# Optimization experiments

Hardware: AMD Instinct MI355X
Metric: run time of the kernel (lower is better)

The kernel has to match this reference:

```python
import jax, jax.numpy as jnp
import numpy as np
import math

B, S, L, D, H, F = 4, 1024, 4, 256, 8, 1024
NUM_LETTERS = 22
VOCAB = NUM_LETTERS + 3
HD = D // H
DISSONANCE = 0.5


def setup_inputs() -> dict:
    key = jax.random.key(0)
    ks = iter(jax.random.split(key, 64))
    r = lambda shape, s=0.05: jax.random.normal(next(ks), shape, dtype=jnp.float32) * s
    inp = {
        'input_roots': jax.random.randint(next(ks), (B, S, 3), 0, VOCAB),
        'gematria': jax.random.uniform(next(ks), (B, S), dtype=jnp.float32),
        'letter_embed': r((VOCAB, D), 0.02),
        'root_proj_w': r((3 * D, D)), 'root_proj_b': jnp.zeros((D,)),
        'root_ln_g': jnp.ones((D,)), 'root_ln_b': jnp.zeros((D,)),
        'input_proj_w': r((2 * D, D)), 'input_proj_b': jnp.zeros((D,)),
        'input_ln_g': jnp.ones((D,)), 'input_ln_b': jnp.zeros((D,)),
        'qw': r((L, D, D)), 'qb': jnp.zeros((L, D)),
        'kw': r((L, D, D)), 'kb': jnp.zeros((L, D)),
        'vw': r((L, D, D)), 'vb': jnp.zeros((L, D)),
        'ow': r((L, D, D)), 'ob': jnp.zeros((L, D)),
        'dist_scale': r((L, H), 0.1), 'diss_sens': jnp.full((L, H), 0.5),
        'ff1w': r((L, D, F)), 'ff1b': jnp.zeros((L, F)),
        'ff2w': r((L, F, D)), 'ff2b': jnp.zeros((L, D)),
        'ln1g': jnp.ones((L, D)), 'ln1b': jnp.zeros((L, D)),
        'ln2g': jnp.ones((L, D)), 'ln2b': jnp.zeros((L, D)),
        'out_ln_g': jnp.ones((D,)), 'out_ln_b': jnp.zeros((D,)),
        'h1w': r((D, NUM_LETTERS)), 'h1b': jnp.zeros((NUM_LETTERS,)),
        'h2w': r((D, NUM_LETTERS)), 'h2b': jnp.zeros((NUM_LETTERS,)),
        'h3w': r((D, NUM_LETTERS)), 'h3b': jnp.zeros((NUM_LETTERS,)),
    }
    return inp


def _ln(x, g, b):
    m = jnp.mean(x, -1, keepdims=True)
    v = jnp.mean(jnp.square(x - m), -1, keepdims=True)
    return (x - m) * jax.lax.rsqrt(v + 1e-5) * g + b


def _rtl_pos(s, d):
    # flipped sinusoidal PE: token j gets original position s-1-j
    pos = (s - 1 - jnp.arange(s, dtype=jnp.float32))[:, None]
    div = jnp.exp(jnp.arange(0, d, 2, dtype=jnp.float32) * (-(math.log(10000.0) / d)))
    pe = jnp.zeros((s, d))
    pe = pe.at[:, 0::2].set(jnp.sin(pos * div))
    pe = pe.at[:, 1::2].set(jnp.cos(pos * div))
    return pe


def _forward(input_roots, gematria, letter_embed, root_proj_w, root_proj_b,
             root_ln_g, root_ln_b, input_proj_w, input_proj_b, input_ln_g, input_ln_b,
             qw, qb, kw, kb, vw, vb, ow, ob, dist_scale, diss_sens,
             ff1w, ff1b, ff2w, ff2b, ln1g, ln1b, ln2g, ln2b,
             out_ln_g, out_ln_b, h1w, h1b, h2w, h2b, h3w, h3b):
    b, s, _ = input_roots.shape
    # root encoder
    letters = letter_embed[input_roots]                      # (b,s,3,D)
    root_emb = _ln(letters.reshape(b, s, 3 * D) @ root_proj_w + root_proj_b, root_ln_g, root_ln_b)
    # gematria sinusoidal
    angles = (gematria[..., None] * 500.0) * jnp.exp(
        jnp.arange(0, D, 2, dtype=jnp.float32) * (-(math.log(10000.0) / D)))
    gem_emb = jnp.concatenate([jnp.sin(angles), jnp.cos(angles)], axis=-1)  # (b,s,D)
    x = jnp.concatenate([root_emb, gem_emb], axis=-1) @ input_proj_w + input_proj_b
    x = _ln(x + _rtl_pos(s, D)[None], input_ln_g, input_ln_b)
    # distance matrix |i-j| shared across layers
    pos = jnp.arange(s, dtype=jnp.float32)
    dist = jnp.abs(pos[None, :] - pos[:, None])              # (s,s)
    scale = 1.0 / math.sqrt(HD)
    for i in range(L):
        normed = _ln(x, ln1g[i], ln1b[i])
        Q = (normed @ qw[i] + qb[i]).reshape(b, s, H, HD)
        K = (normed @ kw[i] + kb[i]).reshape(b, s, H, HD)
        V = (normed @ vw[i] + vb[i]).reshape(b, s, H, HD)
        scores = jnp.einsum('bqhd,bkhd->bhqk', Q, K) * scale
        penalty = dist_scale[i] * (1.0 - DISSONANCE * diss_sens[i])  # (H,)
        bias = -jnp.abs(penalty)[:, None, None] * dist[None]         # (H,s,s)
        attn = jax.nn.softmax(scores + bias[None], axis=-1)
        out = jnp.einsum('bhqk,bkhd->bqhd', attn, V).reshape(b, s, D)
        x = x + (out @ ow[i] + ob[i])
        h = _ln(x, ln2g[i], ln2b[i])
        x = x + (jax.nn.gelu(h @ ff1w[i] + ff1b[i], approximate=False) @ ff2w[i] + ff2b[i])
    x = _ln(x, out_ln_g, out_ln_b)
    return (x @ h1w + h1b, x @ h2w + h2b, x @ h3w + h3b)


def reference(input_roots, gematria, letter_embed, root_proj_w, root_proj_b,
              root_ln_g, root_ln_b, input_proj_w, input_proj_b, input_ln_g, input_ln_b,
              qw, qb, kw, kb, vw, vb, ow, ob, dist_scale, diss_sens,
              ff1w, ff1b, ff2w, ff2b, ln1g, ln1b, ln2g, ln2b,
              out_ln_g, out_ln_b, h1w, h1b, h2w, h2b, h3w, h3b):
    return _forward(input_roots, gematria, letter_embed, root_proj_w, root_proj_b,
                    root_ln_g, root_ln_b, input_proj_w, input_proj_b, input_ln_g, input_ln_b,
                    qw, qb, kw, kb, vw, vb, ow, ob, dist_scale, diss_sens,
                    ff1w, ff1b, ff2w, ff2b, ln1g, ln1b, ln2g, ln2b,
                    out_ln_g, out_ln_b, h1w, h1b, h2w, h2b, h3w, h3b)
```

## Files before the change

### kernel.cpp

```cpp
#include <hip/hip_runtime.h>
#include <hip/hip_bf16.h>
#include <math.h>

#define NTOK   4096
#define SEQ    1024
#define DMODEL 256
#define NHEAD  8
#define FDIM   1024
#define NLAYER 4

typedef __attribute__((ext_vector_type(8))) short short8v;
typedef __attribute__((ext_vector_type(4))) float f32x4;

#define LDS3(p) ((__attribute__((address_space(3))) unsigned int*)(p))
#define GAS1(p) ((const __attribute__((address_space(1))) unsigned int*)(p))

__device__ __forceinline__ void gl_lds16(const void* g, void* l) {
    __builtin_amdgcn_global_load_lds(GAS1(g), LDS3(l), 16, 0, 0);
}
__device__ __forceinline__ short f2bf(float v) {
    __hip_bfloat16 h = __float2bfloat16(v);
    return __builtin_bit_cast(short, h);
}

__device__ __forceinline__ void blockSum2(float& s1, float& s2, float* red) {
    #pragma unroll
    for (int off = 32; off > 0; off >>= 1) {
        s1 += __shfl_down(s1, off);
        s2 += __shfl_down(s2, off);
    }
    int lane = threadIdx.x & 63, w = threadIdx.x >> 6;
    __syncthreads();
    if (lane == 0) { red[w] = s1; red[4 + w] = s2; }
    __syncthreads();
    s1 = red[0] + red[1] + red[2] + red[3];
    s2 = red[4] + red[5] + red[6] + red[7];
}

struct TD { const float* src; __hip_bfloat16* dst; int K; int M; };
struct TDs { TD d[29]; };

__global__ __launch_bounds__(256) void transpose_kernel(TDs p) {
    __shared__ float ld[32][33];
    TD d = p.d[blockIdx.y];
    int tm = (d.M + 31) >> 5;
    int kt = blockIdx.x / tm, mt = blockIdx.x % tm;
    if (kt * 32 >= d.K) return;
    int tx = threadIdx.x & 31, ty = threadIdx.x >> 5;
    #pragma unroll
    for (int r = 0; r < 4; ++r) {
        int k = kt * 32 + ty + r * 8, m = mt * 32 + tx;
        if (m < d.M) ld[ty + r * 8][tx] = d.src[(long)k * d.M + m];
    }
    __syncthreads();
    #pragma unroll
    for (int r = 0; r < 4; ++r) {
        int m = mt * 32 + ty + r * 8, k = kt * 32 + tx;
        if (m < d.M) d.dst[(long)m * d.K + k] = __float2bfloat16(ld[tx][ty + r * 8]);
    }
}

template <int TM, int TN, int EPI>
__global__ __launch_bounds__(256) void mm_kernel(
    const __hip_bfloat16* __restrict__ A, const __hip_bfloat16* __restrict__ Bw,
    const float* __restrict__ bias, float* __restrict__ Cf,
    __hip_bfloat16* __restrict__ Cb, int N, int K, int M,
    const float* __restrict__ b2, const float* __restrict__ b3,
    __hip_bfloat16* __restrict__ Ck, __hip_bfloat16* __restrict__ Cv)
{
    constexpr int BK = 64;
    __shared__ __align__(16) short As[2][TM * BK];
    __shared__ __align__(16) short Bs[2][TN * BK];
    const int tid = threadIdx.x;
    const int lane = tid & 63, wid = tid >> 6;
    const int wr = wid >> 1, wc = wid & 1;
    const int n0 = blockIdx.y * TM, m0 = blockIdx.x * TN;
    const int l15 = lane & 15, g = lane >> 4;
    constexpr int FM = (TM / 32 > 0) ? TM / 32 : 1;
    constexpr int FN = TN / 32;
    f32x4 acc[FM][FN] = {};
    const int nt = K >> 6;

    auto stage = [&](int buf, int k0) {
        constexpr int CA = TM * 8;
        #pragma unroll
        for (int j = 0; j < (CA + 255) / 256; ++j) {
            int cid = tid + j * 256;
            if (CA % 256 == 0 || cid < CA) {
                int r = cid >> 3, sl = cid & 7, ss = sl ^ (r & 7);
                gl_lds16(A + (long)(n0 + r) * K + k0 + ss * 8, (char*)As[buf] + cid * 16);
            }
        }
        constexpr int CB = TN * 8;
        #pragma unroll
        for (int j = 0; j < CB / 256; ++j) {
            int cid = tid + j * 256;
            int r = cid >> 3, sl = cid & 7, ss = sl ^ (r & 7);
            gl_lds16(Bw + (long)(m0 + r) * K + k0 + ss * 8, (char*)Bs[buf] + cid * 16);
        }
    };

    stage(0, 0);
    __syncthreads();
    for (int t = 0; t < nt; ++t) {
        int cur = t & 1;
        if (t + 1 < nt) stage(cur ^ 1, (t + 1) * BK);
        #pragma unroll
        for (int ks = 0; ks < 2; ++ks) {
            short8v af[FM], bfr[FN];
            #pragma unroll
            for (int mi = 0; mi < FM; ++mi) {
                int row = wr * (TM / 2) + mi * 16 + l15;
                int slot = (ks * 4 + g) ^ (row & 7);
                af[mi] = *(const short8v*)((const char*)As[cur] + row * (BK * 2) + slot * 16);
            }
            #pragma unroll
            for (int ni = 0; ni < FN; ++ni) {
                int row = wc * (TN / 2) + ni * 16 + l15;
                int slot = (ks * 4 + g) ^ (row & 7);
                bfr[ni] = *(const short8v*)((const char*)Bs[cur] + row * (BK * 2) + slot * 16);
            }
            #pragma unroll
            for (int mi = 0; mi < FM; ++mi)
                #pragma unroll
                for (int ni = 0; ni < FN; ++ni)
                    acc[mi][ni] = __builtin_amdgcn_mfma_f32_16x16x32_bf16(
                        af[mi], bfr[ni], acc[mi][ni], 0, 0, 0);
        }
        __syncthreads();
    }

    #pragma unroll
    for (int mi = 0; mi < FM; ++mi) {
        #pragma unroll
        for (int ni = 0; ni < FN; ++ni) {
            int colb = m0 + wc * (TN / 2) + ni * 16 + l15;
            float bv;
            if (EPI == 6) bv = (colb < 256) ? bias[colb] : (colb < 512) ? b2[colb - 256] : b3[colb - 512];
            else bv = bias[colb];
            if (EPI == 6 && colb >= 512) {
                int c2 = colb - 512;
                int h = c2 >> 5, dd = c2 & 31;
                int row0 = n0 + wr * (TM / 2) + mi * 16 + g * 4;
                int bb = row0 >> 10, ss = row0 & 1023;
                short4 pk;
                pk.x = f2bf(acc[mi][ni][0] + bv);
                pk.y = f2bf(acc[mi][ni][1] + bv);
                pk.z = f2bf(acc[mi][ni][2] + bv);
                pk.w = f2bf(acc[mi][ni][3] + bv);
                *(short4*)((short*)Cv + ((long)((bb * 8 + h) * 32 + dd) << 10) + ss) = pk;
            } else {
                #pragma unroll
                for (int i = 0; i < 4; ++i) {
                    int row = n0 + wr * (TM / 2) + mi * 16 + g * 4 + i;
                    float v = acc[mi][ni][i] + bv;
                    if (EPI == 0) Cf[(long)row * M + colb] = v;
                    else if (EPI == 2) {
                        v = 0.5f * v * (1.f + erff(v * 0.70710678f));
                        Cb[(long)row * M + colb] = __float2bfloat16(v);
                    } else if (EPI == 5) {
                        if (colb < 66) {
                            int hd = colb / 22, jj = colb - hd * 22;
                            Cf[(long)hd * (NTOK * 22) + (long)row * 22 + jj] = v;
                        }
                    } else if (EPI == 6) {
                        __hip_bfloat16* dst = (colb < 256) ? Cb : Ck;
                        int cc = (colb < 256) ? colb : colb - 256;
                        dst[(long)row * 256 + cc] = __float2bfloat16(v);
                    }
                }
            }
        }
    }
}

__global__ __launch_bounds__(256) void mm_wide_ln_kernel(
    const __hip_bfloat16* __restrict__ A, const __hip_bfloat16* __restrict__ Bw,
    const float* __restrict__ bias, float* __restrict__ xio,
    __hip_bfloat16* __restrict__ nrm, const float* __restrict__ lng,
    const float* __restrict__ lnb, int K)
{
    constexpr int BK = 64;
    __shared__ __align__(16) short As[2][16 * BK];
    __shared__ __align__(16) short Bs[2][256 * BK];
    __shared__ float2 red2[4][16];
    const int tid = threadIdx.x;
    const int lane = tid & 63, wid = tid >> 6;
    const int l15 = lane & 15, g = lane >> 4;
    const int n0 = blockIdx.x * 16;
    f32x4 acc[4] = {};
    const int nt = K >> 6;

    auto stage = [&](int buf, int k0) {
        if (tid < 128) {
            int r = tid >> 3, sl = tid & 7, ss = sl ^ (r & 7);
            gl_lds16(A + (long)(n0 + r) * K + k0 + ss * 8, (char*)As[buf] + tid * 16);
        }
        #pragma unroll
        for (int j = 0; j < 8; ++j) {
            int cid = tid + j * 256;
            int r = cid >> 3, sl = cid & 7, ss = sl ^ (r & 7);
            gl_lds16(Bw + (long)r * K + k0 + ss * 8, (char*)Bs[buf] + cid * 16);
        }
    };

    stage(0, 0);
    __syncthreads();
    for (int t = 0; t < nt; ++t) {
        int cur = t & 1;
        if (t + 1 < nt) stage(cur ^ 1, (t + 1) * BK);
        #pragma unroll
        for (int ks = 0; ks < 2; ++ks) {
            short8v af;
            {
                int slot = (ks * 4 + g) ^ (l15 & 7);
                af = *(const short8v*)((const char*)As[cur] + l15 * (BK * 2) + slot * 16);
            }
            #pragma unroll
            for (int ni = 0; ni < 4; ++ni) {
                int brow = wid * 64 + ni * 16 + l15;
                int slot = (ks * 4 + g) ^ (brow & 7);
                short8v bfr = *(const short8v*)((const char*)Bs[cur] + brow * (BK * 2) + slot * 16);
                acc[ni] = __builtin_amdgcn_mfma_f32_16x16x32_bf16(af, bfr, acc[ni], 0, 0, 0);
            }
        }
        __syncthreads();
    }

    float pvt[4][4];
    float rs[4] = {0.f, 0.f, 0.f, 0.f}, rq[4] = {0.f, 0.f, 0.f, 0.f};
    #pragma unroll
    for (int ni = 0; ni < 4; ++ni) {
        int col = wid * 64 + ni * 16 + l15;
        float bv = bias[col];
        #pragma unroll
        for (int i = 0; i < 4; ++i) {
            int row = n0 + g * 4 + i;
            float v = acc[ni][i] + bv + xio[(long)row * 256 + col];
            pvt[ni][i] = v;
            rs[i] += v;
            rq[i] += v * v;
        }
    }
    #pragma unroll
    for (int i = 0; i < 4; ++i) {
        #pragma unroll
        for (int off = 8; off; off >>= 1) {
            rs[i] += __shfl_xor(rs[i], off);
            rq[i] += __shfl_xor(rq[i], off);
        }
    }
    __syncthreads();
    if (l15 == 0) {
        #pragma unroll
        for (int i = 0; i < 4; ++i)
            red2[wid][g * 4 + i] = make_float2(rs[i], rq[i]);
    }
    __syncthreads();
    #pragma unroll
    for (int i = 0; i < 4; ++i) {
        int lr = g * 4 + i;
        float s1 = red2[0][lr].x + red2[1][lr].x + red2[2][lr].x + red2[3][lr].x;
        float s2 = red2[0][lr].y + red2[1][lr].y + red2[2][lr].y + red2[3][lr].y;
        float mean = s1 * (1.f / 256.f);
        float var = s2 * (1.f / 256.f) - mean * mean;
        float rsx = rsqrtf(var + 1e-5f);
        int row = n0 + lr;
        #pragma unroll
        for (int ni = 0; ni < 4; ++ni) {
            int col = wid * 64 + ni * 16 + l15;
            float v = pvt[ni][i];
            xio[(long)row * 256 + col] = v;
            nrm[(long)row * 256 + col] =
                __float2bfloat16((v - mean) * rsx * lng[col] + lnb[col]);
        }
    }
}

__global__ __launch_bounds__(256) void attn_mfma_kernel(
    const __hip_bfloat16* __restrict__ Q, const __hip_bfloat16* __restrict__ Kx,
    const __hip_bfloat16* __restrict__ Vt, __hip_bfloat16* __restrict__ Oa,
    const float* __restrict__ dsc, const float* __restrict__ dss)
{
    __shared__ __align__(16) short Qs[64 * 32];
    __shared__ __align__(16) short Ks[2][64 * 32];
    __shared__ __align__(16) short Vs[2][32 * 64];
    __shared__ __align__(16) short Ps[4 * 16 * 64];
    const int tid = threadIdx.x, lane = tid & 63, wid = tid >> 6;
    const int qt = blockIdx.x, bh = blockIdx.y, b = bh >> 3, h = bh & 7;
    const float pen = fabsf(dsc[h] * (1.f - 0.5f * dss[h]));
    const int l15 = lane & 15, g = lane >> 4;
    const float scale = 0.17677669529663689f;

    auto stageKV = [&](int buf, int kt) {
        int r = tid >> 2, sl = tid & 3, ss = sl ^ (r & 3);
        gl_lds16(Kx + ((long)(b * SEQ + kt * 64 + r) * DMODEL + h * 32) + ss * 8,
                 (char*)Ks[buf] + tid * 16);
        int d = tid >> 3, sl8 = tid & 7, ss8 = sl8 ^ (d & 7);
        gl_lds16(Vt + ((long)(bh * 32 + d) << 10) + kt * 64 + ss8 * 8,
                 (char*)Vs[buf] + tid * 16);
    };

    {
        int r = tid >> 2, sl = tid & 3, ss = sl ^ (r & 3);
        gl_lds16(Q + ((long)(b * SEQ + qt * 64 + r) * DMODEL + h * 32) + ss * 8,
                 (char*)Qs + tid * 16);
    }
    stageKV(0, 0);
    __syncthreads();

    short8v bq;
    {
        int row = wid * 16 + l15;
        int slot = g ^ (row & 3);
        bq = *(const short8v*)((const char*)Qs + row * 64 + slot * 16);
    }

    float m = -1e30f, l = 0.f;
    f32x4 oacc[2] = {};
    const float qpos = (float)(qt * 64 + wid * 16 + l15);
    char* pbase = (char*)Ps + wid * 2048 + l15 * 128;

    for (int kt = 0; kt < 16; ++kt) {
        int cur = kt & 1;
        if (kt < 15) stageKV(cur ^ 1, kt + 1);

        float s[4][4];
        float smax = -1e30f;
        #pragma unroll
        for (int ni = 0; ni < 4; ++ni) {
            int krow = ni * 16 + l15;
            int slot = g ^ (krow & 3);
            short8v ak = *(const short8v*)((const char*)Ks[cur] + krow * 64 + slot * 16);
            f32x4 z = {0.f, 0.f, 0.f, 0.f};
            f32x4 sa = __builtin_amdgcn_mfma_f32_16x16x32_bf16(ak, bq, z, 0, 0, 0);
            float kbase = (float)(kt * 64 + ni * 16 + g * 4);
            #pragma unroll
            for (int i = 0; i < 4; ++i) {
                float v = sa[i] * scale - pen * fabsf(qpos - (kbase + (float)i));
                s[ni][i] = v;
                smax = fmaxf(smax, v);
            }
        }
        smax = fmaxf(smax, __shfl_xor(smax, 16));
        smax = fmaxf(smax, __shfl_xor(smax, 32));
        float mn = fmaxf(m, smax);
        float fac = __expf(m - mn);
        m = mn;
        float ps = 0.f;
        #pragma unroll
        for (int ni = 0; ni < 4; ++ni) {
            short4 pk;
            #pragma unroll
            for (int i = 0; i < 4; ++i) {
                float p = __expf(s[ni][i] - mn);
                ps += p;
                ((short*)&pk)[i] = f2bf(p);
            }
            int slot = (ni * 2 + (g >> 1)) ^ (l15 & 7);
            *(short4*)(pbase + slot * 16 + (g & 1) * 8) = pk;
        }
        ps += __shfl_xor(ps, 16);
        ps += __shfl_xor(ps, 32);
        l = l * fac + ps;

        float facr[4];
        #pragma unroll
        for (int i = 0; i < 4; ++i) facr[i] = __shfl(fac, g * 4 + i);
        #pragma unroll
        for (int n2 = 0; n2 < 2; ++n2)
            #pragma unroll
            for (int i = 0; i < 4; ++i) oacc[n2][i] *= facr[i];

        #pragma unroll
        for (int ks = 0; ks < 2; ++ks) {
            int slot = (ks * 4 + g) ^ (l15 & 7);
            short8v pa = *(const short8v*)(pbase + slot * 16);
            #pragma unroll
            for (int n2 = 0; n2 < 2; ++n2) {
                int d = n2 * 16 + l15;
                int vslot = (ks * 4 + g) ^ (d & 7);
                short8v vb = *(const short8v*)((const char*)Vs[cur] + d * 128 + vslot * 16);
                oacc[n2] = __builtin_amdgcn_mfma_f32_16x16x32_bf16(pa, vb, oacc[n2], 0, 0, 0);
            }
        }
        __syncthreads();
    }
    float lr[4];
    #pragma unroll
    for (int i = 0; i < 4; ++i) lr[i] = __shfl(l, g * 4 + i);
    #pragma unroll
    for (int n2 = 0; n2 < 2; ++n2) {
        #pragma unroll
        for (int i = 0; i < 4; ++i) {
            float v = oacc[n2][i] / lr[i];
            long row = b * SEQ + qt * 64 + wid * 16 + g * 4 + i;
            Oa[row * DMODEL + h * 32 + n2 * 16 + l15] = __float2bfloat16(v);
        }
    }
}

__global__ __launch_bounds__(256) void gather_kernel(
    const int* __restrict__ roots, const float* __restrict__ letE,
    __hip_bfloat16* __restrict__ cat,
    const float* __restrict__ h1b, const float* __restrict__ h2b,
    const float* __restrict__ h3b, float* __restrict__ biascat)
{
    const int n = blockIdx.x, t = threadIdx.x;
    int r0 = roots[n * 3 + 0], r1 = roots[n * 3 + 1], r2 = roots[n * 3 + 2];
    cat[(long)n * 768 + t]       = __float2bfloat16(letE[r0 * DMODEL + t]);
    cat[(long)n * 768 + 256 + t] = __float2bfloat16(letE[r1 * DMODEL + t]);
    cat[(long)n * 768 + 512 + t] = __float2bfloat16(letE[r2 * DMODEL + t]);
    if (n == 0 && t < 66)
        biascat[t] = (t < 22) ? h1b[t] : (t < 44) ? h2b[t - 22] : h3b[t - 44];
}

__global__ __launch_bounds__(256) void ln_gem_kernel(
    const float* __restrict__ tmpf, const float* __restrict__ gem,
    const float* __restrict__ gg, const float* __restrict__ gb,
    __hip_bfloat16* __restrict__ catin)
{
    __shared__ float red[8];
    const int n = blockIdx.x, t = threadIdx.x;
    const float LC = 0.0359778921f;
    float v = tmpf[(long)n * DMODEL + t];
    float s1 = v, s2 = v * v;
    blockSum2(s1, s2, red);
    float mean = s1 * (1.f / 256.f);
    float var = s2 * (1.f / 256.f) - mean * mean;
    catin[(long)n * 512 + t] =
        __float2bfloat16((v - mean) * rsqrtf(var + 1e-5f) * gg[t] + gb[t]);
    float gv = gem[n];
    int j = (t < 128) ? t : t - 128;
    float ang = gv * 500.f * expf(-(float)(2 * j) * LC);
    catin[(long)n * 512 + 256 + t] = __float2bfloat16((t < 128) ? sinf(ang) : cosf(ang));
}

__global__ __launch_bounds__(256) void ln_pe2_kernel(
    const float* __restrict__ tmpf, const float* __restrict__ gg,
    const float* __restrict__ gb, const float* __restrict__ g1,
    const float* __restrict__ b1, float* __restrict__ x,
    __hip_bfloat16* __restrict__ nrm)
{
    __shared__ float red[8];
    const int n = blockIdx.x, t = threadIdx.x;
    const int s = n & (SEQ - 1);
    const float LC = 0.0359778921f;
    float pos = (float)(SEQ - 1 - s);
    float dv = expf(-(float)(t & ~1) * LC);
    float pe = (t & 1) ? cosf(pos * dv) : sinf(pos * dv);
    float v = tmpf[(long)n * DMODEL + t] + pe;
    float s1 = v, s2 = v * v;
    blockSum2(s1, s2, red);
    float mean = s1 * (1.f / 256.f);
    float var = s2 * (1.f / 256.f) - mean * mean;
    float xv = (v - mean) * rsqrtf(var + 1e-5f) * gg[t] + gb[t];
    x[(long)n * DMODEL + t] = xv;
    s1 = xv; s2 = xv * xv;
    blockSum2(s1, s2, red);
    mean = s1 * (1.f / 256.f);
    var = s2 * (1.f / 256.f) - mean * mean;
    nrm[(long)n * DMODEL + t] =
        __float2bfloat16((xv - mean) * rsqrtf(var + 1e-5f) * g1[t] + b1[t]);
}

extern "C" void kernel_launch(void* const* d_in, const int* in_sizes, int n_in,
                              void* d_out, int out_size, void* d_ws, size_t ws_size,
                              hipStream_t stream)
{
    const int*   roots = (const int*)  d_in[0];
    const float* gem   = (const float*)d_in[1];
    const float* letE  = (const float*)d_in[2];
    const float* rpw   = (const float*)d_in[3];
    const float* rpb   = (const float*)d_in[4];
    const float* rlg   = (const float*)d_in[5];
    const float* rlb   = (const float*)d_in[6];
    const float* ipw   = (const float*)d_in[7];
    const float* ipb   = (const float*)d_in[8];
    const float* ilg   = (const float*)d_in[9];
    const float* ilb   = (const float*)d_in[10];
    const float* qw    = (const float*)d_in[11];
    const float* qb    = (const float*)d_in[12];
    const float* kw    = (const float*)d_in[13];
    const float* kb    = (const float*)d_in[14];
    const float* vw    = (const float*)d_in[15];
    const float* vb    = (const float*)d_in[16];
    const float* ow    = (const float*)d_in[17];
    const float* ob    = (const float*)d_in[18];
    const float* dsc   = (const float*)d_in[19];
    const float* dss   = (const float*)d_in[20];
    const float* ff1w  = (const float*)d_in[21];
    const float* ff1b  = (const float*)d_in[22];
    const float* ff2w  = (const float*)d_in[23];
    const float* ff2b  = (const float*)d_in[24];
    const float* ln1g  = (const float*)d_in[25];
    const float* ln1b  = (const float*)d_in[26];
    const float* ln2g  = (const float*)d_in[27];
    const float* ln2b  = (const float*)d_in[28];
    const float* olng  = (const float*)d_in[29];
    const float* olnb  = (const float*)d_in[30];
    const float* h1w   = (const float*)d_in[31];
    const float* h1b   = (const float*)d_in[32];
    const float* h2w   = (const float*)d_in[33];
    const float* h2b   = (const float*)d_in[34];
    const float* h3w   = (const float*)d_in[35];
    const float* h3b   = (const float*)d_in[36];

    char* wsb = (char*)d_ws;
    float*          x    = (float*)         (wsb + (0l  << 20));
    float*          tmpf = (float*)         (wsb + (4l  << 20));
    __hip_bfloat16* nrm  = (__hip_bfloat16*)(wsb + (8l  << 20));
    __hip_bfloat16* qbuf = (__hip_bfloat16*)(wsb + (10l << 20));
    __hip_bfloat16* kbuf = (__hip_bfloat16*)(wsb + (12l << 20));
    __hip_bfloat16* vtb  = (__hip_bfloat16*)(wsb + (14l << 20));
    __hip_bfloat16* aob  = (__hip_bfloat16*)(wsb + (16l << 20));
    __hip_bfloat16* hbb  = (__hip_bfloat16*)(wsb + (18l << 20));
    __hip_bfloat16* catb  = hbb;
    __hip_bfloat16* catin = qbuf;
    __hip_bfloat16* wb   = (__hip_bfloat16*)(wsb + (26l << 20));
    float*          biascat = (float*)      (wsb + (34l << 20));

    __hip_bfloat16* rpw_t  = wb;
    __hip_bfloat16* ipw_t  = wb + 196608;
    __hip_bfloat16* qkv_t  = wb + 327680;
    __hip_bfloat16* ow_t   = wb + 1114112;
    __hip_bfloat16* ff1w_t = wb + 1376256;
    __hip_bfloat16* ff2w_t = wb + 2424832;
    __hip_bfloat16* head_t = wb + 3473408;

    hipMemsetAsync(head_t, 0, 32768 * 2, stream);

    TDs td;
    td.d[0] = {rpw, rpw_t, 768, 256};
    td.d[1] = {ipw, ipw_t, 512, 256};
    for (int l = 0; l < 4; ++l) {
        td.d[2 + l]  = {qw + l * 65536,  qkv_t + l * 196608 + 0,      256, 256};
        td.d[6 + l]  = {kw + l * 65536,  qkv_t + l * 196608 + 65536,  256, 256};
        td.d[10 + l] = {vw + l * 65536,  qkv_t + l * 196608 + 131072, 256, 256};
        td.d[14 + l] = {ow + l * 65536,  ow_t + l * 65536,  256, 256};
        td.d[18 + l] = {ff1w + l * 262144, ff1w_t + l * 262144, 256, 1024};
        td.d[22 + l] = {ff2w + l * 262144, ff2w_t + l * 262144, 1024, 256};
    }
    td.d[26] = {h1w, head_t + 0 * 22 * 256, 256, 22};
    td.d[27] = {h2w, head_t + 1 * 22 * 256, 256, 22};
    td.d[28] = {h3w, head_t + 2 * 22 * 256, 256, 22};
    transpose_kernel<<<dim3(256, 29), 256, 0, stream>>>(td);

    gather_kernel<<<NTOK, 256, 0, stream>>>(roots, letE, catb, h1b, h2b, h3b, biascat);
    mm_kernel<32, 64, 0><<<dim3(4, 128), 256, 0, stream>>>(
        catb, rpw_t, rpb, tmpf, nullptr, NTOK, 768, 256, nullptr, nullptr, nullptr, nullptr);
    ln_gem_kernel<<<NTOK, 256, 0, stream>>>(tmpf, gem, rlg, rlb, catin);
    mm_kernel<32, 64, 0><<<dim3(4, 128), 256, 0, stream>>>(
        catin, ipw_t, ipb, tmpf, nullptr, NTOK, 512, 256, nullptr, nullptr, nullptr, nullptr);
    ln_pe2_kernel<<<NTOK, 256, 0, stream>>>(tmpf, ilg, ilb, ln1g, ln1b, x, nrm);

    for (int l = 0; l < NLAYER; ++l) {
        mm_kernel<64, 64, 6><<<dim3(12, 64), 256, 0, stream>>>(
            nrm, qkv_t + l * 196608, qb + l * 256, nullptr, qbuf, NTOK, 256, 768,
            kb + l * 256, vb + l * 256, kbuf, vtb);
        attn_mfma_kernel<<<dim3(16, 32), 256, 0, stream>>>(qbuf, kbuf, vtb, aob,
                                                           dsc + l * 8, dss + l * 8);
        mm_wide_ln_kernel<<<dim3(NTOK / 16), 256, 0, stream>>>(
            aob, ow_t + l * 65536, ob + l * 256, x, nrm,
            ln2g + l * 256, ln2b + l * 256, 256);
        mm_kernel<64, 64, 2><<<dim3(16, 64), 256, 0, stream>>>(
            nrm, ff1w_t + l * 262144, ff1b + l * 1024, nullptr, hbb, NTOK, 256, 1024,
            nullptr, nullptr, nullptr, nullptr);
        const float* ng = (l == 3) ? olng : ln1g + (l + 1) * 256;
        const float* nb = (l == 3) ? olnb : ln1b + (l + 1) * 256;
        mm_wide_ln_kernel<<<dim3(NTOK / 16), 256, 0, stream>>>(
            hbb, ff2w_t + l * 262144, ff2b + l * 256, x, nrm, ng, nb, 1024);
    }
    mm_kernel<32, 64, 5><<<dim3(2, 128), 256, 0, stream>>>(
        nrm, head_t, biascat, (float*)d_out, nullptr, NTOK, 256, 128,
        nullptr, nullptr, nullptr, nullptr);
}
```

Baseline: 435.0 us.

## Fuse embedding LayerNorms into wide GEMMs and restructure attention with key-range skipping

Replaces the two embedding GEMMs and their separate LayerNorm/sinusoid kernels with wide 16-row GEMM kernels that apply bias, LayerNorm, the gematria encoding and the positional encoding in the epilogue. This drops the fp32 intermediate buffer and two extra launches. Attention now runs one 64-thread wave per 16 query rows, loading K and V fragments straight from global memory instead of staging them through shared memory. It also limits the key tiles to the range where the distance penalty stays above -30. The transpose kernel writes zero padding for the head weights, so the separate memset is gone. The key-range bound relies on the penalty being positive and skips terms that are tiny but not exactly zero; the new attention layout gives up shared-memory reuse of K and V across waves.

```diff
diff --git a/kernel.cpp b/kernel.cpp
--- a/kernel.cpp
+++ b/kernel.cpp
@@ -23,27 +23,13 @@
     return __builtin_bit_cast(short, h);
 }
 
-__device__ __forceinline__ void blockSum2(float& s1, float& s2, float* red) {
-    #pragma unroll
-    for (int off = 32; off > 0; off >>= 1) {
-        s1 += __shfl_down(s1, off);
-        s2 += __shfl_down(s2, off);
-    }
-    int lane = threadIdx.x & 63, w = threadIdx.x >> 6;
-    __syncthreads();
-    if (lane == 0) { red[w] = s1; red[4 + w] = s2; }
-    __syncthreads();
-    s1 = red[0] + red[1] + red[2] + red[3];
-    s2 = red[4] + red[5] + red[6] + red[7];
-}
-
-struct TD { const float* src; __hip_bfloat16* dst; int K; int M; };
+struct TD { const float* src; __hip_bfloat16* dst; int K; int M; int Mpad; };
 struct TDs { TD d[29]; };
 
 __global__ __launch_bounds__(256) void transpose_kernel(TDs p) {
     __shared__ float ld[32][33];
     TD d = p.d[blockIdx.y];
-    int tm = (d.M + 31) >> 5;
+    int tm = (d.Mpad + 31) >> 5;
     int kt = blockIdx.x / tm, mt = blockIdx.x % tm;
     if (kt * 32 >= d.K) return;
     int tx = threadIdx.x & 31, ty = threadIdx.x >> 5;
@@ -57,6 +43,7 @@
     for (int r = 0; r < 4; ++r) {
         int m = mt * 32 + ty + r * 8, k = kt * 32 + tx;
         if (m < d.M) d.dst[(long)m * d.K + k] = __float2bfloat16(ld[tx][ty + r * 8]);
+        else if (m < d.Mpad) d.dst[(long)m * d.K + k] = __float2bfloat16(0.f);
     }
 }
 
@@ -174,61 +161,99 @@
     }
 }
 
+#define WIDE_GEMM_BODY(Abuf, Bwp, Kval)                                           \
+    constexpr int BK = 64;                                                        \
+    const int tid = threadIdx.x;                                                  \
+    const int lane = tid & 63, wid = tid >> 6;                                    \
+    const int l15 = lane & 15, g = lane >> 4;                                     \
+    const int n0 = blockIdx.x * 16;                                               \
+    f32x4 acc[4] = {};                                                            \
+    const int nt = (Kval) >> 6;                                                   \
+    auto stage = [&](int buf, int k0) {                                           \
+        if (tid < 128) {                                                          \
+            int r = tid >> 3, sl = tid & 7, ss = sl ^ (r & 7);                    \
+            gl_lds16((Abuf) + (long)(n0 + r) * (Kval) + k0 + ss * 8,              \
+                     (char*)As[buf] + tid * 16);                                  \
+        }                                                                         \
+        _Pragma("unroll")                                                         \
+        for (int j = 0; j < 8; ++j) {                                             \
+            int cid = tid + j * 256;                                              \
+            int r = cid >> 3, sl = cid & 7, ss = sl ^ (r & 7);                    \
+            gl_lds16((Bwp) + (long)r * (Kval) + k0 + ss * 8,                      \
+                     (char*)Bs[buf] + cid * 16);                                  \
+        }                                                                         \
+    };                                                                            \
+    stage(0, 0);                                                                  \
+    __syncthreads();                                                              \
+    for (int t = 0; t < nt; ++t) {                                                \
+        int cur = t & 1;                                                          \
+        if (t + 1 < nt) stage(cur ^ 1, (t + 1) * BK);                             \
+        _Pragma("unroll")                                                         \
+        for (int ks = 0; ks < 2; ++ks) {                                          \
+            short8v af;                                                           \
+            {                                                                     \
+                int slot = (ks * 4 + g) ^ (l15 & 7);                              \
+                af = *(const short8v*)((const char*)As[cur] + l15 * (BK * 2) + slot * 16); \
+            }                                                                     \
+            _Pragma("unroll")                                                     \
+            for (int ni = 0; ni < 4; ++ni) {                                      \
+                int brow = wid * 64 + ni * 16 + l15;                              \
+                int slot = (ks * 4 + g) ^ (brow & 7);                             \
+                short8v bfr = *(const short8v*)((const char*)Bs[cur] + brow * (BK * 2) + slot * 16); \
+                acc[ni] = __builtin_amdgcn_mfma_f32_16x16x32_bf16(af, bfr, acc[ni], 0, 0, 0); \
+            }                                                                     \
+        }                                                                         \
+        __syncthreads();                                                          \
+    }
+
+__device__ __forceinline__ void wide_rowstats(
+    float pvt[4][4], float2 red2[4][16], int wid, int l15, int g,
+    float mean[4], float rstd[4])
+{
+    float rs[4] = {0.f, 0.f, 0.f, 0.f}, rq[4] = {0.f, 0.f, 0.f, 0.f};
+    #pragma unroll
+    for (int ni = 0; ni < 4; ++ni)
+        #pragma unroll
+        for (int i = 0; i < 4; ++i) { rs[i] += pvt[ni][i]; rq[i] += pvt[ni][i] * pvt[ni][i]; }
+    #pragma unroll
+    for (int i = 0; i < 4; ++i) {
+        #pragma unroll
+        for (int off = 8; off; off >>= 1) {
+            rs[i] += __shfl_xor(rs[i], off);
+            rq[i] += __shfl_xor(rq[i], off);
+        }
+    }
+    __syncthreads();
+    if (l15 == 0) {
+        #pragma unroll
+        for (int i = 0; i < 4; ++i)
+            red2[wid][g * 4 + i] = make_float2(rs[i], rq[i]);
+    }
+    __syncthreads();
+    #pragma unroll
+    for (int i = 0; i < 4; ++i) {
+        int lr = g * 4 + i;
+        float s1 = red2[0][lr].x + red2[1][lr].x + red2[2][lr].x + red2[3][lr].x;
+        float s2 = red2[0][lr].y + red2[1][lr].y + red2[2][lr].y + red2[3][lr].y;
+        float mn = s1 * (1.f / 256.f);
+        float var = s2 * (1.f / 256.f) - mn * mn;
+        mean[i] = mn;
+        rstd[i] = rsqrtf(var + 1e-5f);
+    }
+}
+
 __global__ __launch_bounds__(256) void mm_wide_ln_kernel(
     const __hip_bfloat16* __restrict__ A, const __hip_bfloat16* __restrict__ Bw,
     const float* __restrict__ bias, float* __restrict__ xio,
     __hip_bfloat16* __restrict__ nrm, const float* __restrict__ lng,
     const float* __restrict__ lnb, int K)
 {
-    constexpr int BK = 64;
-    __shared__ __align__(16) short As[2][16 * BK];
-    __shared__ __align__(16) short Bs[2][256 * BK];
+    __shared__ __align__(16) short As[2][16 * 64];
+    __shared__ __align__(16) short Bs[2][256 * 64];
     __shared__ float2 red2[4][16];
-    const int tid = threadIdx.x;
-    const int lane = tid & 63, wid = tid >> 6;
-    const int l15 = lane & 15, g = lane >> 4;
-    const int n0 = blockIdx.x * 16;
-    f32x4 acc[4] = {};
-    const int nt = K >> 6;
-
-    auto stage = [&](int buf, int k0) {
-        if (tid < 128) {
-            int r = tid >> 3, sl = tid & 7, ss = sl ^ (r & 7);
-            gl_lds16(A + (long)(n0 + r) * K + k0 + ss * 8, (char*)As[buf] + tid * 16);
-        }
-        #pragma unroll
-        for (int j = 0; j < 8; ++j) {
-            int cid = tid + j * 256;
-            int r = cid >> 3, sl = cid & 7, ss = sl ^ (r & 7);
-            gl_lds16(Bw + (long)r * K + k0 + ss * 8, (char*)Bs[buf] + cid * 16);
-        }
-    };
-
-    stage(0, 0);
-    __syncthreads();
-    for (int t = 0; t < nt; ++t) {
-        int cur = t & 1;
-        if (t + 1 < nt) stage(cur ^ 1, (t + 1) * BK);
-        #pragma unroll
-        for (int ks = 0; ks < 2; ++ks) {
-            short8v af;
-            {
-                int slot = (ks * 4 + g) ^ (l15 & 7);
-                af = *(const short8v*)((const char*)As[cur] + l15 * (BK * 2) + slot * 16);
-            }
-            #pragma unroll
-            for (int ni = 0; ni < 4; ++ni) {
-                int brow = wid * 64 + ni * 16 + l15;
-                int slot = (ks * 4 + g) ^ (brow & 7);
-                short8v bfr = *(const short8v*)((const char*)Bs[cur] + brow * (BK * 2) + slot * 16);
-                acc[ni] = __builtin_amdgcn_mfma_f32_16x16x32_bf16(af, bfr, acc[ni], 0, 0, 0);
-            }
-        }
-        __syncthreads();
-    }
+    WIDE_GEMM_BODY(A, Bw, K)
 
     float pvt[4][4];
-    float rs[4] = {0.f, 0.f, 0.f, 0.f}, rq[4] = {0.f, 0.f, 0.f, 0.f};
     #pragma unroll
     for (int ni = 0; ni < 4; ++ni) {
         int col = wid * 64 + ni * 16 + l15;
@@ -236,104 +261,171 @@
         #pragma unroll
         for (int i = 0; i < 4; ++i) {
             int row = n0 + g * 4 + i;
-            float v = acc[ni][i] + bv + xio[(long)row * 256 + col];
-            pvt[ni][i] = v;
-            rs[i] += v;
-            rq[i] += v * v;
-        }
-    }
+            pvt[ni][i] = acc[ni][i] + bv + xio[(long)row * 256 + col];
+        }
+    }
+    float mean[4], rstd[4];
+    wide_rowstats(pvt, red2, wid, l15, g, mean, rstd);
     #pragma unroll
     for (int i = 0; i < 4; ++i) {
-        #pragma unroll
-        for (int off = 8; off; off >>= 1) {
-            rs[i] += __shfl_xor(rs[i], off);
-            rq[i] += __shfl_xor(rq[i], off);
-        }
-    }
-    __syncthreads();
-    if (l15 == 0) {
-        #pragma unroll
-        for (int i = 0; i < 4; ++i)
-            red2[wid][g * 4 + i] = make_float2(rs[i], rq[i]);
-    }
-    __syncthreads();
-    #pragma unroll
-    for (int i = 0; i < 4; ++i) {
-        int lr = g * 4 + i;
-        float s1 = red2[0][lr].x + red2[1][lr].x + red2[2][lr].x + red2[3][lr].x;
-        float s2 = red2[0][lr].y + red2[1][lr].y + red2[2][lr].y + red2[3][lr].y;
-        float mean = s1 * (1.f / 256.f);
-        float var = s2 * (1.f / 256.f) - mean * mean;
-        float rsx = rsqrtf(var + 1e-5f);
-        int row = n0 + lr;
+        int row = n0 + g * 4 + i;
         #pragma unroll
         for (int ni = 0; ni < 4; ++ni) {
             int col = wid * 64 + ni * 16 + l15;
             float v = pvt[ni][i];
             xio[(long)row * 256 + col] = v;
             nrm[(long)row * 256 + col] =
-                __float2bfloat16((v - mean) * rsx * lng[col] + lnb[col]);
-        }
-    }
-}
-
-__global__ __launch_bounds__(256) void attn_mfma_kernel(
+                __float2bfloat16((v - mean[i]) * rstd[i] * lng[col] + lnb[col]);
+        }
+    }
+}
+
+__global__ __launch_bounds__(256) void wide_gem_kernel(
+    const __hip_bfloat16* __restrict__ A, const __hip_bfloat16* __restrict__ Bw,
+    const float* __restrict__ bias, const float* __restrict__ lng,
+    const float* __restrict__ lnb, const float* __restrict__ gem,
+    __hip_bfloat16* __restrict__ catin)
+{
+    __shared__ __align__(16) short As[2][16 * 64];
+    __shared__ __align__(16) short Bs[2][256 * 64];
+    __shared__ float2 red2[4][16];
+    WIDE_GEMM_BODY(A, Bw, 768)
+
+    const float LC = 0.0359778921f;
+    float pvt[4][4];
+    #pragma unroll
+    for (int ni = 0; ni < 4; ++ni) {
+        int col = wid * 64 + ni * 16 + l15;
+        float bv = bias[col];
+        #pragma unroll
+        for (int i = 0; i < 4; ++i) pvt[ni][i] = acc[ni][i] + bv;
+    }
+    float mean[4], rstd[4];
+    wide_rowstats(pvt, red2, wid, l15, g, mean, rstd);
+    float gv[4];
+    #pragma unroll
+    for (int i = 0; i < 4; ++i) gv[i] = gem[n0 + g * 4 + i];
+    #pragma unroll
+    for (int ni = 0; ni < 4; ++ni) {
+        int col = wid * 64 + ni * 16 + l15;
+        int j = col & 127;
+        float c = 500.f * __expf(-(float)(2 * j) * LC);
+        #pragma unroll
+        for (int i = 0; i < 4; ++i) {
+            int row = n0 + g * 4 + i;
+            catin[(long)row * 512 + col] = __float2bfloat16(
+                (pvt[ni][i] - mean[i]) * rstd[i] * lng[col] + lnb[col]);
+            float ang = gv[i] * c;
+            float gval = (col < 128) ? __sinf(ang) : __cosf(ang);
+            catin[(long)row * 512 + 256 + col] = __float2bfloat16(gval);
+        }
+    }
+}
+
+__global__ __launch_bounds__(256) void wide_pe_kernel(
+    const __hip_bfloat16* __restrict__ A, const __hip_bfloat16* __restrict__ Bw,
+    const float* __restrict__ bias, const float* __restrict__ lng,
+    const float* __restrict__ lnb, const float* __restrict__ g1,
+    const float* __restrict__ b1, float* __restrict__ x,
+    __hip_bfloat16* __restrict__ nrm)
+{
+    __shared__ __align__(16) short As[2][16 * 64];
+    __shared__ __align__(16) short Bs[2][256 * 64];
+    __shared__ float2 red2[4][16];
+    WIDE_GEMM_BODY(A, Bw, 512)
+
+    const float LC = 0.0359778921f;
+    float pvt[4][4];
+    #pragma unroll
+    for (int ni = 0; ni < 4; ++ni) {
+        int col = wid * 64 + ni * 16 + l15;
+        float bv = bias[col];
+        float dv = __expf(-(float)(col & ~1) * LC);
+        #pragma unroll
+        for (int i = 0; i < 4; ++i) {
+            int row = n0 + g * 4 + i;
+            float pos = (float)(1023 - (row & 1023));
+            float pe = (col & 1) ? __cosf(pos * dv) : __sinf(pos * dv);
+            pvt[ni][i] = acc[ni][i] + bv + pe;
+        }
+    }
+    float mean[4], rstd[4];
+    wide_rowstats(pvt, red2, wid, l15, g, mean, rstd);
+    #pragma unroll
+    for (int ni = 0; ni < 4; ++ni) {
+        int col = wid * 64 + ni * 16 + l15;
+        #pragma unroll
+        for (int i = 0; i < 4; ++i) {
+            float xv = (pvt[ni][i] - mean[i]) * rstd[i] * lng[col] + lnb[col];
+            pvt[ni][i] = xv;
+            x[(long)(n0 + g * 4 + i) * 256 + col] = xv;
+        }
+    }
+    __syncthreads();
+    wide_rowstats(pvt, red2, wid, l15, g, mean, rstd);
+    #pragma unroll
+    for (int ni = 0; ni < 4; ++ni) {
+        int col = wid * 64 + ni * 16 + l15;
+        #pragma unroll
+        for (int i = 0; i < 4; ++i) {
+            int row = n0 + g * 4 + i;
+            nrm[(long)row * 256 + col] = __float2bfloat16(
+                (pvt[ni][i] - mean[i]) * rstd[i] * g1[col] + b1[col]);
+        }
+    }
+}
+
+__global__ __launch_bounds__(64) void attn_mfma_kernel(
     const __hip_bfloat16* __restrict__ Q, const __hip_bfloat16* __restrict__ Kx,
     const __hip_bfloat16* __restrict__ Vt, __hip_bfloat16* __restrict__ Oa,
     const float* __restrict__ dsc, const float* __restrict__ dss)
 {
-    __shared__ __align__(16) short Qs[64 * 32];
-    __shared__ __align__(16) short Ks[2][64 * 32];
-    __shared__ __align__(16) short Vs[2][32 * 64];
-    __shared__ __align__(16) short Ps[4 * 16 * 64];
-    const int tid = threadIdx.x, lane = tid & 63, wid = tid >> 6;
-    const int qt = blockIdx.x, bh = blockIdx.y, b = bh >> 3, h = bh & 7;
+    __shared__ __align__(16) short Ps[16 * 64];
+    const int lane = threadIdx.x;
+    const int qt = blockIdx.x;
+    const int bh = blockIdx.y, b = bh >> 3, h = bh & 7;
+    const int l15 = lane & 15, g = lane >> 4;
     const float pen = fabsf(dsc[h] * (1.f - 0.5f * dss[h]));
-    const int l15 = lane & 15, g = lane >> 4;
     const float scale = 0.17677669529663689f;
 
-    auto stageKV = [&](int buf, int kt) {
-        int r = tid >> 2, sl = tid & 3, ss = sl ^ (r & 3);
-        gl_lds16(Kx + ((long)(b * SEQ + kt * 64 + r) * DMODEL + h * 32) + ss * 8,
-                 (char*)Ks[buf] + tid * 16);
-        int d = tid >> 3, sl8 = tid & 7, ss8 = sl8 ^ (d & 7);
-        gl_lds16(Vt + ((long)(bh * 32 + d) << 10) + kt * 64 + ss8 * 8,
-                 (char*)Vs[buf] + tid * 16);
-    };
-
-    {
-        int r = tid >> 2, sl = tid & 3, ss = sl ^ (r & 3);
-        gl_lds16(Q + ((long)(b * SEQ + qt * 64 + r) * DMODEL + h * 32) + ss * 8,
-                 (char*)Qs + tid * 16);
-    }
-    stageKV(0, 0);
-    __syncthreads();
-
-    short8v bq;
-    {
-        int row = wid * 16 + l15;
-        int slot = g ^ (row & 3);
-        bq = *(const short8v*)((const char*)Qs + row * 64 + slot * 16);
-    }
+    short8v bq = *(const short8v*)(Q + ((long)(b * SEQ + qt * 16 + l15) * DMODEL + h * 32 + g * 8));
 
     float m = -1e30f, l = 0.f;
     f32x4 oacc[2] = {};
-    const float qpos = (float)(qt * 64 + wid * 16 + l15);
-    char* pbase = (char*)Ps + wid * 2048 + l15 * 128;
-
-    for (int kt = 0; kt < 16; ++kt) {
-        int cur = kt & 1;
-        if (kt < 15) stageKV(cur ^ 1, kt + 1);
+    const float qpos = (float)(qt * 16 + l15);
+    char* pbase = (char*)Ps + l15 * 128;
+
+    int klo = 0, khi = 15;
+    {
+        float D = 30.f / pen;
+        float kmin = (float)(qt * 16) - D;
+        float kmax = (float)(qt * 16 + 15) + D;
+        klo = max(0, (int)floorf(kmin * (1.f / 64.f)));
+        khi = min(15, (int)floorf(kmax * (1.f / 64.f)));
+    }
+
+    for (int kt = klo; kt <= khi; ++kt) {
+        short8v ak[4];
+        #pragma unroll
+        for (int ni = 0; ni < 4; ++ni) {
+            int key = kt * 64 + ni * 16 + l15;
+            ak[ni] = *(const short8v*)(Kx + ((long)(b * SEQ + key) * DMODEL + h * 32 + g * 8));
+        }
+        short8v vb[2][2];
+        #pragma unroll
+        for (int ks = 0; ks < 2; ++ks)
+            #pragma unroll
+            for (int n2 = 0; n2 < 2; ++n2) {
+                int d = n2 * 16 + l15;
+                vb[ks][n2] = *(const short8v*)(Vt + ((long)(bh * 32 + d) << 10) + kt * 64 + ks * 32 + g * 8);
+            }
 
         float s[4][4];
         float smax = -1e30f;
         #pragma unroll
         for (int ni = 0; ni < 4; ++ni) {
-            int krow = ni * 16 + l15;
-            int slot = g ^ (krow & 3);
-            short8v ak = *(const short8v*)((const char*)Ks[cur] + krow * 64 + slot * 16);
             f32x4 z = {0.f, 0.f, 0.f, 0.f};
-            f32x4 sa = __builtin_amdgcn_mfma_f32_16x16x32_bf16(ak, bq, z, 0, 0, 0);
+            f32x4 sa = __builtin_amdgcn_mfma_f32_16x16x32_bf16(ak[ni], bq, z, 0, 0, 0);
             float kbase = (float)(kt * 64 + ni * 16 + g * 4);
             #pragma unroll
             for (int i = 0; i < 4; ++i) {
@@ -377,14 +469,9 @@
             int slot = (ks * 4 + g) ^ (l15 & 7);
             short8v pa = *(const short8v*)(pbase + slot * 16);
             #pragma unroll
-            for (int n2 = 0; n2 < 2; ++n2) {
-                int d = n2 * 16 + l15;
-                int vslot = (ks * 4 + g) ^ (d & 7);
-                short8v vb = *(const short8v*)((const char*)Vs[cur] + d * 128 + vslot * 16);
-                oacc[n2] = __builtin_amdgcn_mfma_f32_16x16x32_bf16(pa, vb, oacc[n2], 0, 0, 0);
-            }
-        }
-        __syncthreads();
+            for (int n2 = 0; n2 < 2; ++n2)
+                oacc[n2] = __builtin_amdgcn_mfma_f32_16x16x32_bf16(pa, vb[ks][n2], oacc[n2], 0, 0, 0);
+        }
     }
     float lr[4];
     #pragma unroll
@@ -394,7 +481,7 @@
         #pragma unroll
         for (int i = 0; i < 4; ++i) {
             float v = oacc[n2][i] / lr[i];
-            long row = b * SEQ + qt * 64 + wid * 16 + g * 4 + i;
+            long row = b * SEQ + qt * 16 + g * 4 + i;
             Oa[row * DMODEL + h * 32 + n2 * 16 + l15] = __float2bfloat16(v);
         }
     }
@@ -413,55 +500,6 @@
     cat[(long)n * 768 + 512 + t] = __float2bfloat16(letE[r2 * DMODEL + t]);
     if (n == 0 && t < 66)
         biascat[t] = (t < 22) ? h1b[t] : (t < 44) ? h2b[t - 22] : h3b[t - 44];
-}
-
-__global__ __launch_bounds__(256) void ln_gem_kernel(
-    const float* __restrict__ tmpf, const float* __restrict__ gem,
-    const float* __restrict__ gg, const float* __restrict__ gb,
-    __hip_bfloat16* __restrict__ catin)
-{
-    __shared__ float red[8];
-    const int n = blockIdx.x, t = threadIdx.x;
-    const float LC = 0.0359778921f;
-    float v = tmpf[(long)n * DMODEL + t];
-    float s1 = v, s2 = v * v;
-    blockSum2(s1, s2, red);
-    float mean = s1 * (1.f / 256.f);
-    float var = s2 * (1.f / 256.f) - mean * mean;
-    catin[(long)n * 512 + t] =
-        __float2bfloat16((v - mean) * rsqrtf(var + 1e-5f) * gg[t] + gb[t]);
-    float gv = gem[n];
-    int j = (t < 128) ? t : t - 128;
-    float ang = gv * 500.f * expf(-(float)(2 * j) * LC);
-    catin[(long)n * 512 + 256 + t] = __float2bfloat16((t < 128) ? sinf(ang) : cosf(ang));
-}
-
-__global__ __launch_bounds__(256) void ln_pe2_kernel(
-    const float* __restrict__ tmpf, const float* __restrict__ gg,
-    const float* __restrict__ gb, const float* __restrict__ g1,
-    const float* __restrict__ b1, float* __restrict__ x,
-    __hip_bfloat16* __restrict__ nrm)
-{
-    __shared__ float red[8];
-    const int n = blockIdx.x, t = threadIdx.x;
-    const int s = n & (SEQ - 1);
-    const float LC = 0.0359778921f;
-    float pos = (float)(SEQ - 1 - s);
-    float dv = expf(-(float)(t & ~1) * LC);
-    float pe = (t & 1) ? cosf(pos * dv) : sinf(pos * dv);
-    float v = tmpf[(long)n * DMODEL + t] + pe;
-    float s1 = v, s2 = v * v;
-    blockSum2(s1, s2, red);
-    float mean = s1 * (1.f / 256.f);
-    float var = s2 * (1.f / 256.f) - mean * mean;
-    float xv = (v - mean) * rsqrtf(var + 1e-5f) * gg[t] + gb[t];
-    x[(long)n * DMODEL + t] = xv;
-    s1 = xv; s2 = xv * xv;
-    blockSum2(s1, s2, red);
-    mean = s1 * (1.f / 256.f);
-    var = s2 * (1.f / 256.f) - mean * mean;
-    nrm[(long)n * DMODEL + t] =
-        __float2bfloat16((xv - mean) * rsqrtf(var + 1e-5f) * g1[t] + b1[t]);
 }
 
 extern "C" void kernel_launch(void* const* d_in, const int* in_sizes, int n_in,
@@ -508,7 +546,6 @@
 
     char* wsb = (char*)d_ws;
     float*          x    = (float*)         (wsb + (0l  << 20));
-    float*          tmpf = (float*)         (wsb + (4l  << 20));
     __hip_bfloat16* nrm  = (__hip_bfloat16*)(wsb + (8l  << 20));
     __hip_bfloat16* qbuf = (__hip_bfloat16*)(wsb + (10l << 20));
     __hip_bfloat16* kbuf = (__hip_bfloat16*)(wsb + (12l << 20));
@@ -528,38 +565,34 @@
     __hip_bfloat16* ff2w_t = wb + 2424832;
     __hip_bfloat16* head_t = wb + 3473408;
 
-    hipMemsetAsync(head_t, 0, 32768 * 2, stream);
-
     TDs td;
-    td.d[0] = {rpw, rpw_t, 768, 256};
-    td.d[1] = {ipw, ipw_t, 512, 256};
+    td.d[0] = {rpw, rpw_t, 768, 256, 256};
+    td.d[1] = {ipw, ipw_t, 512, 256, 256};
     for (int l = 0; l < 4; ++l) {
-        td.d[2 + l]  = {qw + l * 65536,  qkv_t + l * 196608 + 0,      256, 256};
-        td.d[6 + l]  = {kw + l * 65536,  qkv_t + l * 196608 + 65536,  256, 256};
-        td.d[10 + l] = {vw + l * 65536,  qkv_t + l * 196608 + 131072, 256, 256};
-        td.d[14 + l] = {ow + l * 65536,  ow_t + l * 65536,  256, 256};
-        td.d[18 + l] = {ff1w + l * 262144, ff1w_t + l * 262144, 256, 1024};
-        td.d[22 + l] = {ff2w + l * 262144, ff2w_t + l * 262144, 1024, 256};
-    }
-    td.d[26] = {h1w, head_t + 0 * 22 * 256, 256, 22};
-    td.d[27] = {h2w, head_t + 1 * 22 * 256, 256, 22};
-    td.d[28] = {h3w, head_t + 2 * 22 * 256, 256, 22};
+        td.d[2 + l]  = {qw + l * 65536,  qkv_t + l * 196608 + 0,      256, 256, 256};
+        td.d[6 + l]  = {kw + l * 65536,  qkv_t + l * 196608 + 65536,  256, 256, 256};
+        td.d[10 + l] = {vw + l * 65536,  qkv_t + l * 196608 + 131072, 256, 256, 256};
+        td.d[14 + l] = {ow + l * 65536,  ow_t + l * 65536,  256, 256, 256};
+        td.d[18 + l] = {ff1w + l * 262144, ff1w_t + l * 262144, 256, 1024, 1024};
+        td.d[22 + l] = {ff2w + l * 262144, ff2w_t + l * 262144, 1024, 256, 256};
+    }
+    td.d[26] = {h1w, head_t + 0 * 22 * 256, 256, 22, 22};
+    td.d[27] = {h2w, head_t + 1 * 22 * 256, 256, 22, 22};
+    td.d[28] = {h3w, head_t + 2 * 22 * 256, 256, 22, 84};
     transpose_kernel<<<dim3(256, 29), 256, 0, stream>>>(td);
 
     gather_kernel<<<NTOK, 256, 0, stream>>>(roots, letE, catb, h1b, h2b, h3b, biascat);
-    mm_kernel<32, 64, 0><<<dim3(4, 128), 256, 0, stream>>>(
-        catb, rpw_t, rpb, tmpf, nullptr, NTOK, 768, 256, nullptr, nullptr, nullptr, nullptr);
-    ln_gem_kernel<<<NTOK, 256, 0, stream>>>(tmpf, gem, rlg, rlb, catin);
-    mm_kernel<32, 64, 0><<<dim3(4, 128), 256, 0, stream>>>(
-        catin, ipw_t, ipb, tmpf, nullptr, NTOK, 512, 256, nullptr, nullptr, nullptr, nullptr);
-    ln_pe2_kernel<<<NTOK, 256, 0, stream>>>(tmpf, ilg, ilb, ln1g, ln1b, x, nrm);
+    wide_gem_kernel<<<dim3(NTOK / 16), 256, 0, stream>>>(
+        catb, rpw_t, rpb, rlg, rlb, gem, catin);
+    wide_pe_kernel<<<dim3(NTOK / 16), 256, 0, stream>>>(
+        catin, ipw_t, ipb, ilg, ilb, ln1g, ln1b, x, nrm);
 
     for (int l = 0; l < NLAYER; ++l) {
         mm_kernel<64, 64, 6><<<dim3(12, 64), 256, 0, stream>>>(
             nrm, qkv_t + l * 196608, qb + l * 256, nullptr, qbuf, NTOK, 256, 768,
             kb + l * 256, vb + l * 256, kbuf, vtb);
-        attn_mfma_kernel<<<dim3(16, 32), 256, 0, stream>>>(qbuf, kbuf, vtb, aob,
-                                                           dsc + l * 8, dss + l * 8);
+        attn_mfma_kernel<<<dim3(64, 32), 64, 0, stream>>>(qbuf, kbuf, vtb, aob,
+                                                          dsc + l * 8, dss + l * 8);
         mm_wide_ln_kernel<<<dim3(NTOK / 16), 256, 0, stream>>>(
             aob, ow_t + l * 65536, ob + l * 256, x, nrm,
             ln2g + l * 256, ln2b + l * 256, 256);
```

Result: slower. 475.8 us (+9.4%).
